# Kernel optimization log

Hardware: AMD Instinct MI355X
Metric: run time of the kernel (lower is better)

The kernel has to match this reference:

```python
import jax, jax.numpy as jnp
import numpy as np

B, N, E, H = 1, 4096, 2048, 16
D = E // H  # head_size = 128
DEGREE = 4
LN_EPS = 1e-5
ROPE_BASE = 10000.0


def rope_cos_sin(n, d):
    # [n, d//2] tables
    inv_freq = 1.0 / (ROPE_BASE ** (jnp.arange(0, d, 2, dtype=jnp.float32) / d))
    t = jnp.arange(n, dtype=jnp.float32)[:, None] * inv_freq[None, :]
    return jnp.cos(t), jnp.sin(t)


def apply_rope(x, cos, sin):
    # x: [b, n, h, d]; rotate-half RoPE
    x1, x2 = jnp.split(x, 2, axis=-1)
    c = cos[None, :, None, :]
    s = sin[None, :, None, :]
    return jnp.concatenate([x1 * c - x2 * s, x1 * s + x2 * c], axis=-1)


def layernorm(x, scale, bias, eps=LN_EPS):
    m = jnp.mean(x, axis=-1, keepdims=True)
    v = jnp.var(x, axis=-1, keepdims=True)
    return (x - m) * jax.lax.rsqrt(v + eps) * scale + bias


def polynomial_attention(q, k, v, degree, is_causal):
    # q,k,v: [b, h, n, d]
    a = jnp.einsum('bhnd,bhmd->bhnm', q, k) ** degree
    if is_causal:
        a = jnp.tril(a)
    denom = jnp.sum(a, axis=-1, keepdims=True)
    return jnp.einsum('bhnm,bhmd->bhnd', a / denom, v)


def setup_inputs() -> dict:
    key = jax.random.key(0)
    k0, k1, k2 = jax.random.split(key, 3)
    x = jax.random.normal(k0, (B, N, E), dtype=jnp.float32)
    # Dense(3*emb_dim, use_bias=False) and Dense(emb_dim, use_bias=False)
    w_qkv = jax.random.normal(k1, (E, 3 * E), dtype=jnp.float32) * (1.0 / np.sqrt(E))
    w_out = jax.random.normal(k2, (E, E), dtype=jnp.float32) * (1.0 / np.sqrt(E))
    # shared pre-attention LayerNorm over head dim (flax init: scale=1, bias=0)
    ln_scale = jnp.ones((D,), dtype=jnp.float32)
    ln_bias = jnp.zeros((D,), dtype=jnp.float32)
    return {"x": x, "w_qkv": w_qkv, "w_out": w_out,
            "ln_scale": ln_scale, "ln_bias": ln_bias}


def reference(x, w_qkv, w_out, ln_scale, ln_bias):
    b, n, e = x.shape
    proj = x @ w_qkv                              # [b, n, 3e]
    q, k, v = jnp.split(proj, 3, axis=-1)
    q = q.reshape(b, n, H, D)
    k = k.reshape(b, n, H, D)
    v = v.reshape(b, n, H, D)
    cos, sin = rope_cos_sin(n, D)
    q = apply_rope(q, cos, sin)
    k = apply_rope(k, cos, sin)
    # transpose branch (non-softmax): [b, h, n, d]
    q = q.transpose(0, 2, 1, 3)
    k = k.transpose(0, 2, 1, 3)
    v = v.transpose(0, 2, 1, 3)
    # shared pre_attn LayerNorm applied to q and k
    q = layernorm(q, ln_scale, ln_bias)
    k = layernorm(k, ln_scale, ln_bias)
    out = polynomial_attention(q, k, v, DEGREE, True)  # [b, h, n, d]
    out = out.transpose(0, 2, 1, 3).reshape(b, n, e)
    out = out @ w_out                              # dropout rate 0 / inference: identity
    return out
```

## Files before the change

### kernel.cpp

```cpp
#include <hip/hip_runtime.h>
#include <stdint.h>
#include <math.h>

#define N_SEQ 4096
#define EDIM  2048
#define NH    16
#define HD    128

typedef __attribute__((ext_vector_type(8))) short bf16x8;
typedef __attribute__((ext_vector_type(4))) float f32x4;

#define AS1 __attribute__((address_space(1)))
#define AS3 __attribute__((address_space(3)))

__device__ __forceinline__ void gll16(const unsigned short* g, unsigned short* l) {
    __builtin_amdgcn_global_load_lds((const AS1 unsigned int*)g,
                                     (AS3 unsigned int*)l, 16, 0, 0);
}

__device__ __forceinline__ unsigned short f2bf(float f) {
    union { float f; unsigned u; } v; v.f = f;
    unsigned r = v.u + 0x7FFFu + ((v.u >> 16) & 1u);
    return (unsigned short)(r >> 16);
}
__device__ __forceinline__ float bf2f(unsigned short h) {
    union { unsigned u; float f; } v; v.u = ((unsigned)h) << 16;
    return v.f;
}

__global__ void k_convert_x(const float* __restrict__ x,
                            unsigned short* __restrict__ xb, int n4) {
    int i = blockIdx.x * blockDim.x + threadIdx.x;
    int stride = gridDim.x * blockDim.x;
    for (; i < n4; i += stride) {
        float4 v = ((const float4*)x)[i];
        ushort4 o;
        o.x = f2bf(v.x); o.y = f2bf(v.y); o.z = f2bf(v.z); o.w = f2bf(v.w);
        ((ushort4*)xb)[i] = o;
    }
}

__global__ void k_transpose_f32_bf16(const float* __restrict__ in,
                                     unsigned short* __restrict__ out,
                                     int R, int C) {
    __shared__ unsigned short Ls[64][68];
    const int c0 = blockIdx.x * 64, r0 = blockIdx.y * 64;
    const int t = threadIdx.x;
    #pragma unroll
    for (int i = 0; i < 4; ++i) {
        int ch = i * 256 + t;
        int r = ch >> 4, c4 = (ch & 15) * 4;
        float4 v = *(const float4*)&in[(size_t)(r0 + r) * C + c0 + c4];
        ushort4 o;
        o.x = f2bf(v.x); o.y = f2bf(v.y); o.z = f2bf(v.z); o.w = f2bf(v.w);
        *(ushort4*)&Ls[r][c4] = o;
    }
    __syncthreads();
    #pragma unroll
    for (int i = 0; i < 2; ++i) {
        int ch = i * 256 + t;
        int rr = ch >> 3, c8 = (ch & 7) * 8;
        unsigned short vals[8];
        #pragma unroll
        for (int j = 0; j < 8; ++j) vals[j] = Ls[c8 + j][rr];
        uint4 pk;
        pk.x = (unsigned)vals[0] | ((unsigned)vals[1] << 16);
        pk.y = (unsigned)vals[2] | ((unsigned)vals[3] << 16);
        pk.z = (unsigned)vals[4] | ((unsigned)vals[5] << 16);
        pk.w = (unsigned)vals[6] | ((unsigned)vals[7] << 16);
        *(uint4*)&out[(size_t)(c0 + rr) * R + r0 + c8] = pk;
    }
}

template<int F32OUT>
__launch_bounds__(256, 2)
__global__ void k_gemm_bt(const unsigned short* __restrict__ A,
                          const unsigned short* __restrict__ Bt,
                          void* __restrict__ C,
                          int M, int N, int K) {
    __shared__ unsigned short sh[2 * 128 * 64];
    unsigned short* As = sh;
    unsigned short* Bs = sh + 128 * 64;

    const int t = threadIdx.x;
    const int wave = t >> 6, lane = t & 63;
    const int wm = wave >> 1, wn = wave & 1;
    const int lg = lane >> 4, lr = lane & 15;

    const int nbx = gridDim.x;
    const int nwg = nbx * gridDim.y;
    int bid = blockIdx.y * nbx + blockIdx.x;
    int swz = (bid & 7) * (nwg >> 3) + (bid >> 3);
    const int m0 = (swz / nbx) * 128;
    const int n0 = (swz % nbx) * 128;

    const unsigned short* aptr = A  + (size_t)m0 * K;
    const unsigned short* bptr = Bt + (size_t)n0 * K;

    f32x4 acc[4][4];
    #pragma unroll
    for (int i = 0; i < 4; ++i)
        #pragma unroll
        for (int j = 0; j < 4; ++j) acc[i][j] = f32x4{0.f, 0.f, 0.f, 0.f};

    int schr[4], srow[4], scb[4];
    #pragma unroll
    for (int i = 0; i < 4; ++i) {
        int ch = (i * 4 + wave) * 64 + lane;
        schr[i] = ch;
        srow[i] = ch >> 3;
        scb[i]  = (ch & 7) ^ ((ch >> 3) & 7);
    }

    const int nkb = K >> 6;
    for (int kb = 0; kb < nkb; ++kb) {
        __syncthreads();
        #pragma unroll
        for (int i = 0; i < 4; ++i) {
            const size_t goff = (size_t)srow[i] * K + (size_t)kb * 64 + scb[i] * 8;
            gll16(&aptr[goff], &As[schr[i] * 8]);
            gll16(&bptr[goff], &Bs[schr[i] * 8]);
        }
        __syncthreads();

        #pragma unroll
        for (int kk = 0; kk < 2; ++kk) {
            bf16x8 af[4], bf[4];
            const int cbx = ((kk * 4 + lg) ^ (lr & 7)) * 8;
            #pragma unroll
            for (int i = 0; i < 4; ++i) {
                af[i] = *(const bf16x8*)&As[(wm * 64 + i * 16 + lr) * 64 + cbx];
                bf[i] = *(const bf16x8*)&Bs[(wn * 64 + i * 16 + lr) * 64 + cbx];
            }
            #pragma unroll
            for (int i = 0; i < 4; ++i)
                #pragma unroll
                for (int j = 0; j < 4; ++j)
                    acc[i][j] = __builtin_amdgcn_mfma_f32_16x16x32_bf16(af[i], bf[j], acc[i][j], 0, 0, 0);
        }
    }

    if (F32OUT) {
        #pragma unroll
        for (int i = 0; i < 4; ++i) {
            int row0 = m0 + wm * 64 + i * 16 + lg * 4;
            #pragma unroll
            for (int j = 0; j < 4; ++j) {
                int col = n0 + wn * 64 + j * 16 + lr;
                #pragma unroll
                for (int r = 0; r < 4; ++r)
                    ((float*)C)[(size_t)(row0 + r) * N + col] = acc[i][j][r];
            }
        }
    } else {
        __syncthreads();
        unsigned short* Cs = sh;
        #pragma unroll
        for (int i = 0; i < 4; ++i) {
            #pragma unroll
            for (int j = 0; j < 4; ++j) {
                int col = wn * 64 + j * 16 + lr;
                #pragma unroll
                for (int r = 0; r < 4; ++r)
                    Cs[(wm * 64 + i * 16 + lg * 4 + r) * 128 + col] = f2bf(acc[i][j][r]);
            }
        }
        __syncthreads();
        #pragma unroll
        for (int i = 0; i < 8; ++i) {
            int ch = i * 256 + t;
            int row = ch >> 4, c8 = (ch & 15) * 8;
            *(uint4*)&((unsigned short*)C)[(size_t)(m0 + row) * N + n0 + c8] =
                *(const uint4*)&Cs[row * 128 + c8];
        }
    }
}

__global__ void k_ropeln(const unsigned short* __restrict__ proj,
                         const float* __restrict__ ln_scale,
                         const float* __restrict__ ln_bias,
                         unsigned short* __restrict__ Qh,
                         unsigned short* __restrict__ Kh) {
    const int n = blockIdx.x;
    const int wave = threadIdx.x >> 6, lane = threadIdx.x & 63;
    float inv = expf(-((float)(2 * lane) / 128.0f) * 9.210340371976184f);
    float ang = (float)n * inv;
    float c = cosf(ang), s = sinf(ang);
    const float sc1 = ln_scale[lane], sc2 = ln_scale[lane + 64];
    const float b1 = ln_bias[lane],  b2 = ln_bias[lane + 64];

    for (int r = wave; r < 32; r += 4) {
        int h = r >> 1, qk = r & 1;
        const unsigned short* src = proj + (size_t)n * (3 * EDIM) + qk * EDIM + h * HD;
        float x1 = bf2f(src[lane]), x2 = bf2f(src[lane + 64]);
        float o1 = x1 * c - x2 * s;
        float o2 = x1 * s + x2 * c;
        float sum = o1 + o2, sq = o1 * o1 + o2 * o2;
        #pragma unroll
        for (int d = 1; d < 64; d <<= 1) {
            sum += __shfl_xor(sum, d);
            sq  += __shfl_xor(sq, d);
        }
        float mean = sum * (1.0f / 128.0f);
        float var = sq * (1.0f / 128.0f) - mean * mean;
        float rstd = rsqrtf(var + 1e-5f);
        float y1 = (o1 - mean) * rstd * sc1 + b1;
        float y2 = (o2 - mean) * rstd * sc2 + b2;
        unsigned short* dst = (qk ? Kh : Qh) + ((size_t)h * N_SEQ + n) * HD;
        dst[lane]      = f2bf(y1);
        dst[lane + 64] = f2bf(y2);
    }
}

__global__ void k_vtrans(const unsigned short* __restrict__ proj,
                         unsigned short* __restrict__ Vt) {
    __shared__ unsigned short Ls[64][136];
    const int h = blockIdx.y;
    const int n0 = blockIdx.x * 64;
    const int t = threadIdx.x;
    #pragma unroll
    for (int i = 0; i < 4; ++i) {
        int ch = i * 256 + t;
        int r = ch >> 4, d0 = (ch & 15) * 8;
        uint4 v = *(const uint4*)&proj[(size_t)(n0 + r) * (3 * EDIM) + 2 * EDIM + h * HD + d0];
        *(uint4*)&Ls[r][d0] = v;
    }
    __syncthreads();
    #pragma unroll
    for (int i = 0; i < 4; ++i) {
        int ch = i * 256 + t;
        int d = ch >> 3, p = ch & 7;
        unsigned short vals[8];
        #pragma unroll
        for (int j = 0; j < 8; ++j) {
            int ko = 32 * (p >> 2) + 16 * (j >> 2) + 4 * (p & 3) + (j & 3);
            vals[j] = Ls[ko][d];
        }
        uint4 pk;
        pk.x = (unsigned)vals[0] | ((unsigned)vals[1] << 16);
        pk.y = (unsigned)vals[2] | ((unsigned)vals[3] << 16);
        pk.z = (unsigned)vals[4] | ((unsigned)vals[5] << 16);
        pk.w = (unsigned)vals[6] | ((unsigned)vals[7] << 16);
        *(uint4*)&Vt[((size_t)h * HD + d) * N_SEQ + n0 + p * 8] = pk;
    }
}

__launch_bounds__(256, 2)
__global__ void k_attn(const unsigned short* __restrict__ Qh,
                       const unsigned short* __restrict__ Kh,
                       const unsigned short* __restrict__ Vt,
                       unsigned short* __restrict__ O) {
    __shared__ unsigned short pool[4 * 8192];

    const int t = threadIdx.x;
    const int w = t >> 6, lane = t & 63;
    const int wq = w >> 1, wk = w & 1;
    const int lg = lane >> 4, lr = lane & 15;

    const int b = blockIdx.x;
    const int h = (b & 7) * 2 + ((b >> 3) & 1);
    const int qt = 63 - (b >> 4);
    const int q0 = qt * 64;
    const int qbase = q0 + wq * 32;
    const int kbase = wk * 32;

    bf16x8 qf[2][4];
    #pragma unroll
    for (int mi = 0; mi < 2; ++mi)
        #pragma unroll
        for (int kk = 0; kk < 4; ++kk)
            qf[mi][kk] = *(const bf16x8*)&Qh[((size_t)h * N_SEQ + qbase + mi * 16 + lr) * HD + kk * 32 + lg * 8];

    f32x4 acc[2][8];
    #pragma unroll
    for (int i = 0; i < 2; ++i)
        #pragma unroll
        for (int j = 0; j < 8; ++j) acc[i][j] = f32x4{0.f, 0.f, 0.f, 0.f};
    f32x4 accd[2];
    accd[0] = f32x4{0.f, 0.f, 0.f, 0.f};
    accd[1] = f32x4{0.f, 0.f, 0.f, 0.f};

    bf16x8 onesf;
    {
        short ov = (lr == 0) ? (short)0x3F80 : (short)0;
        #pragma unroll
        for (int j = 0; j < 8; ++j) onesf[j] = ov;
    }

    int kch[4], vch[4];
    const unsigned short* kg[4];
    const unsigned short* vg[4];
    #pragma unroll
    for (int i = 0; i < 4; ++i) {
        int ch = i * 256 + t;
        kch[i] = ch;
        int r = ch >> 4, p = ch & 15;
        int csrc = (p & 8) | ((p ^ r) & 7);
        kg[i] = Kh + ((size_t)h * N_SEQ + r) * HD + csrc * 8;
    }
    #pragma unroll
    for (int i = 0; i < 4; ++i) {
        int ch = i * 256 + t;
        vch[i] = ch;
        int d = ch >> 3, p2 = ch & 7;
        int c2src = (p2 ^ d) & 7;
        vg[i] = Vt + ((size_t)h * HD + d) * N_SEQ + c2src * 8;
    }

    const int nkb = qt + 1;

    union U8 { unsigned u[4]; bf16x8 v; };

    auto stage = [&](unsigned short* Kn, unsigned short* Vn) {
        #pragma unroll
        for (int i = 0; i < 4; ++i) { gll16(kg[i], Kn + kch[i] * 8); kg[i] += 64 * HD; }
        #pragma unroll
        for (int i = 0; i < 4; ++i) { gll16(vg[i], Vn + vch[i] * 8); vg[i] += 64; }
    };

    auto compute = [&](int k0, const unsigned short* Kc, const unsigned short* Vc) {
        if (k0 + kbase > qbase + 31) return;
        f32x4 sa[2][2];
        #pragma unroll
        for (int i = 0; i < 2; ++i) {
            sa[i][0] = f32x4{0.f, 0.f, 0.f, 0.f};
            sa[i][1] = f32x4{0.f, 0.f, 0.f, 0.f};
        }
        bf16x8 kf[2][4];
        #pragma unroll
        for (int nj = 0; nj < 2; ++nj)
            #pragma unroll
            for (int kk = 0; kk < 4; ++kk) {
                int row = kbase + nj * 16 + lr;
                int c = kk * 4 + lg;
                int cs = (c & 8) | ((c ^ row) & 7);
                kf[nj][kk] = *(const bf16x8*)&Kc[row * 128 + cs * 8];
            }
        __builtin_amdgcn_s_setprio(1);
        #pragma unroll
        for (int kk = 0; kk < 4; ++kk)
            #pragma unroll
            for (int nj = 0; nj < 2; ++nj)
                #pragma unroll
                for (int mi = 0; mi < 2; ++mi)
                    sa[mi][nj] = __builtin_amdgcn_mfma_f32_16x16x32_bf16(
                        kf[nj][kk], qf[mi][kk], sa[mi][nj], 0, 0, 0);
        __builtin_amdgcn_s_setprio(0);

        unsigned wreg[2][2][2];
        const bool nomask = (k0 + kbase + 31 <= qbase);
        #pragma unroll
        for (int mi = 0; mi < 2; ++mi)
            #pragma unroll
            for (int nj = 0; nj < 2; ++nj) {
                float p[4];
                #pragma unroll
                for (int r = 0; r < 4; ++r) {
                    float sv = sa[mi][nj][r];
                    float t2 = sv * sv;
                    p[r] = t2 * t2;
                    if (!nomask) {
                        int gk = k0 + kbase + nj * 16 + lg * 4 + r;
                        int gq = qbase + mi * 16 + lr;
                        p[r] = (gk <= gq) ? p[r] : 0.0f;
                    }
                }
                asm("v_cvt_pk_bf16_f32 %0, %1, %2" : "=v"(wreg[mi][nj][0]) : "v"(p[0]), "v"(p[1]));
                asm("v_cvt_pk_bf16_f32 %0, %1, %2" : "=v"(wreg[mi][nj][1]) : "v"(p[2]), "v"(p[3]));
            }

        bf16x8 pa[2];
        #pragma unroll
        for (int mi = 0; mi < 2; ++mi) {
            U8 u;
            u.u[0] = wreg[mi][0][0];
            u.u[1] = wreg[mi][0][1];
            u.u[2] = wreg[mi][1][0];
            u.u[3] = wreg[mi][1][1];
            pa[mi] = u.v;
        }
        __builtin_amdgcn_s_setprio(1);
        #pragma unroll
        for (int ni = 0; ni < 8; ++ni) {
            int d = ni * 16 + lr;
            int cs = ((wk * 4 + lg) ^ (d & 7)) & 7;
            bf16x8 vf = *(const bf16x8*)&Vc[d * 64 + cs * 8];
            #pragma unroll
            for (int mi = 0; mi < 2; ++mi)
                acc[mi][ni] = __builtin_amdgcn_mfma_f32_16x16x32_bf16(pa[mi], vf, acc[mi][ni], 0, 0, 0);
        }
        #pragma unroll
        for (int mi = 0; mi < 2; ++mi)
            accd[mi] = __builtin_amdgcn_mfma_f32_16x16x32_bf16(pa[mi], onesf, accd[mi], 0, 0, 0);
        __builtin_amdgcn_s_setprio(0);
    };

    stage(pool, pool + 16384);
    int kb0 = 0;
    if (nkb & 1) {
        asm volatile("s_waitcnt vmcnt(0)" ::: "memory");
        __builtin_amdgcn_s_barrier();
        compute(0, pool, pool + 16384);
        __builtin_amdgcn_s_barrier();
        if (nkb > 1) stage(pool, pool + 16384);
        kb0 = 1;
    }
    for (int kb = kb0; kb < nkb; kb += 2) {
        stage(pool + 8192, pool + 16384 + 8192);
        asm volatile("s_waitcnt vmcnt(8)" ::: "memory");
        __builtin_amdgcn_s_barrier();
        compute(kb * 64, pool, pool + 16384);
        __builtin_amdgcn_s_barrier();
        if (kb + 2 < nkb) {
            stage(pool, pool + 16384);
            asm volatile("s_waitcnt vmcnt(8)" ::: "memory");
        } else {
            asm volatile("s_waitcnt vmcnt(0)" ::: "memory");
        }
        __builtin_amdgcn_s_barrier();
        compute((kb + 1) * 64, pool + 8192, pool + 16384 + 8192);
        __builtin_amdgcn_s_barrier();
    }

    asm volatile("s_waitcnt vmcnt(0)" ::: "memory");
    __syncthreads();
    float* Xf = (float*)pool;
    const int xbase = wq * 4608 + lane * 4;
    if (wk == 1) {
        #pragma unroll
        for (int mi = 0; mi < 2; ++mi) {
            #pragma unroll
            for (int ni = 0; ni < 8; ++ni)
                *(f32x4*)&Xf[xbase + (mi * 8 + ni) * 256] = acc[mi][ni];
            *(f32x4*)&Xf[xbase + (16 + mi) * 256] = accd[mi];
        }
    }
    __syncthreads();
    unsigned short* Cs = pool + 20480;
    if (wk == 0) {
        #pragma unroll
        for (int mi = 0; mi < 2; ++mi) {
            #pragma unroll
            for (int ni = 0; ni < 8; ++ni) {
                f32x4 o = *(const f32x4*)&Xf[xbase + (mi * 8 + ni) * 256];
                acc[mi][ni][0] += o[0]; acc[mi][ni][1] += o[1];
                acc[mi][ni][2] += o[2]; acc[mi][ni][3] += o[3];
            }
            f32x4 od = *(const f32x4*)&Xf[xbase + (16 + mi) * 256];
            accd[mi][0] += od[0]; accd[mi][1] += od[1];
            accd[mi][2] += od[2]; accd[mi][3] += od[3];
        }
        #pragma unroll
        for (int mi = 0; mi < 2; ++mi) {
            #pragma unroll
            for (int r = 0; r < 4; ++r) {
                float dv = __shfl(accd[mi][r], lane & 48);
                float rinv = 1.0f / dv;
                int rw = wq * 32 + mi * 16 + lg * 4 + r;
                #pragma unroll
                for (int ni = 0; ni < 8; ++ni)
                    Cs[rw * 128 + ni * 16 + lr] = f2bf(acc[mi][ni][r] * rinv);
            }
        }
    }
    __syncthreads();
    #pragma unroll
    for (int i = 0; i < 4; ++i) {
        int ch = i * 256 + t;
        int row = ch >> 4, c8 = (ch & 15) * 8;
        *(uint4*)&O[(size_t)(q0 + row) * EDIM + h * HD + c8] = *(const uint4*)&Cs[row * 128 + c8];
    }
}

extern "C" void kernel_launch(void* const* d_in, const int* in_sizes, int n_in,
                              void* d_out, int out_size, void* d_ws, size_t ws_size,
                              hipStream_t stream) {
    const float* x        = (const float*)d_in[0];
    const float* w_qkv    = (const float*)d_in[1];
    const float* w_out    = (const float*)d_in[2];
    const float* ln_scale = (const float*)d_in[3];
    const float* ln_bias  = (const float*)d_in[4];

    if (ws_size < 134217728u) return;

    char* ws = (char*)d_ws;
    unsigned short* xb    = (unsigned short*)(ws);
    unsigned short* wqkvT = (unsigned short*)(ws + 16777216);
    unsigned short* woutT = (unsigned short*)(ws + 41943040);
    unsigned short* proj  = (unsigned short*)(ws + 50331648);
    unsigned short* Kh    = (unsigned short*)(ws + 100663296);
    unsigned short* Vt    = (unsigned short*)(ws + 117440512);
    unsigned short* Qh    = wqkvT;
    unsigned short* attnO = xb;

    k_convert_x<<<2048, 256, 0, stream>>>(x, xb, (N_SEQ * EDIM) / 4);
    k_transpose_f32_bf16<<<dim3(3 * EDIM / 64, EDIM / 64), 256, 0, stream>>>(w_qkv, wqkvT, EDIM, 3 * EDIM);
    k_transpose_f32_bf16<<<dim3(EDIM / 64, EDIM / 64), 256, 0, stream>>>(w_out, woutT, EDIM, EDIM);
    k_gemm_bt<0><<<dim3(3 * EDIM / 128, N_SEQ / 128), 256, 0, stream>>>(xb, wqkvT, proj, N_SEQ, 3 * EDIM, EDIM);
    k_ropeln<<<N_SEQ, 256, 0, stream>>>(proj, ln_scale, ln_bias, Qh, Kh);
    k_vtrans<<<dim3(N_SEQ / 64, NH), 256, 0, stream>>>(proj, Vt);
    k_attn<<<1024, 256, 0, stream>>>(Qh, Kh, Vt, attnO);
    k_gemm_bt<1><<<dim3(EDIM / 128, N_SEQ / 128), 256, 0, stream>>>(attnO, woutT, (float*)d_out, N_SEQ, EDIM, EDIM);
}
```

Baseline: 286.3 us.

## Double attention query tile to 128 rows and reorder block scheduling

The attention kernel now processes 128 query rows per block (64 per wave pair) instead of 64, halving the grid to 512 blocks and reusing each staged K/V tile across twice as many queries. Block order is split into two batches, the first longest-first and the second shortest-first, to balance causal work across CUs. The cross-wave reduction is done in two passes to fit the larger accumulator set in LDS. The cost is much higher register pressure from doubled accumulators and Q fragments, which may lower occupancy under the 2-blocks launch bound.

```diff
diff --git a/kernel.cpp b/kernel.cpp
--- a/kernel.cpp
+++ b/kernel.cpp
@@ -257,28 +257,30 @@
     const int wq = w >> 1, wk = w & 1;
     const int lg = lane >> 4, lr = lane & 15;
 
-    const int b = blockIdx.x;
-    const int h = (b & 7) * 2 + ((b >> 3) & 1);
-    const int qt = 63 - (b >> 4);
-    const int q0 = qt * 64;
-    const int qbase = q0 + wq * 32;
+    const int s = blockIdx.x & 255;
+    const int batch = blockIdx.x >> 8;
+    const int h = (s & 7) * 2 + ((s >> 3) & 1);
+    const int qq = s >> 4;
+    const int qt = batch ? qq : (31 - qq);
+    const int q0 = qt * 128;
+    const int qbase = q0 + wq * 64;
     const int kbase = wk * 32;
 
-    bf16x8 qf[2][4];
-    #pragma unroll
-    for (int mi = 0; mi < 2; ++mi)
+    bf16x8 qf[4][4];
+    #pragma unroll
+    for (int mi = 0; mi < 4; ++mi)
         #pragma unroll
         for (int kk = 0; kk < 4; ++kk)
             qf[mi][kk] = *(const bf16x8*)&Qh[((size_t)h * N_SEQ + qbase + mi * 16 + lr) * HD + kk * 32 + lg * 8];
 
-    f32x4 acc[2][8];
-    #pragma unroll
-    for (int i = 0; i < 2; ++i)
+    f32x4 acc[4][8];
+    #pragma unroll
+    for (int i = 0; i < 4; ++i)
         #pragma unroll
         for (int j = 0; j < 8; ++j) acc[i][j] = f32x4{0.f, 0.f, 0.f, 0.f};
-    f32x4 accd[2];
-    accd[0] = f32x4{0.f, 0.f, 0.f, 0.f};
-    accd[1] = f32x4{0.f, 0.f, 0.f, 0.f};
+    f32x4 accd[4];
+    #pragma unroll
+    for (int i = 0; i < 4; ++i) accd[i] = f32x4{0.f, 0.f, 0.f, 0.f};
 
     bf16x8 onesf;
     {
@@ -307,7 +309,7 @@
         vg[i] = Vt + ((size_t)h * HD + d) * N_SEQ + c2src * 8;
     }
 
-    const int nkb = qt + 1;
+    const int nkb = 2 * qt + 2;
 
     union U8 { unsigned u[4]; bf16x8 v; };
 
@@ -319,38 +321,37 @@
     };
 
     auto compute = [&](int k0, const unsigned short* Kc, const unsigned short* Vc) {
-        if (k0 + kbase > qbase + 31) return;
-        f32x4 sa[2][2];
-        #pragma unroll
-        for (int i = 0; i < 2; ++i) {
+        if (k0 + kbase > qbase + 63) return;
+        f32x4 sa[4][2];
+        #pragma unroll
+        for (int i = 0; i < 4; ++i) {
             sa[i][0] = f32x4{0.f, 0.f, 0.f, 0.f};
             sa[i][1] = f32x4{0.f, 0.f, 0.f, 0.f};
         }
-        bf16x8 kf[2][4];
-        #pragma unroll
-        for (int nj = 0; nj < 2; ++nj)
+        #pragma unroll
+        for (int nj = 0; nj < 2; ++nj) {
+            bf16x8 kf4[4];
             #pragma unroll
             for (int kk = 0; kk < 4; ++kk) {
                 int row = kbase + nj * 16 + lr;
                 int c = kk * 4 + lg;
                 int cs = (c & 8) | ((c ^ row) & 7);
-                kf[nj][kk] = *(const bf16x8*)&Kc[row * 128 + cs * 8];
-            }
-        __builtin_amdgcn_s_setprio(1);
-        #pragma unroll
-        for (int kk = 0; kk < 4; ++kk)
-            #pragma unroll
-            for (int nj = 0; nj < 2; ++nj)
-                #pragma unroll
-                for (int mi = 0; mi < 2; ++mi)
+                kf4[kk] = *(const bf16x8*)&Kc[row * 128 + cs * 8];
+            }
+            __builtin_amdgcn_s_setprio(1);
+            #pragma unroll
+            for (int kk = 0; kk < 4; ++kk)
+                #pragma unroll
+                for (int mi = 0; mi < 4; ++mi)
                     sa[mi][nj] = __builtin_amdgcn_mfma_f32_16x16x32_bf16(
-                        kf[nj][kk], qf[mi][kk], sa[mi][nj], 0, 0, 0);
-        __builtin_amdgcn_s_setprio(0);
-
-        unsigned wreg[2][2][2];
+                        kf4[kk], qf[mi][kk], sa[mi][nj], 0, 0, 0);
+            __builtin_amdgcn_s_setprio(0);
+        }
+
+        unsigned wreg[4][2][2];
         const bool nomask = (k0 + kbase + 31 <= qbase);
         #pragma unroll
-        for (int mi = 0; mi < 2; ++mi)
+        for (int mi = 0; mi < 4; ++mi)
             #pragma unroll
             for (int nj = 0; nj < 2; ++nj) {
                 float p[4];
@@ -369,9 +370,9 @@
                 asm("v_cvt_pk_bf16_f32 %0, %1, %2" : "=v"(wreg[mi][nj][1]) : "v"(p[2]), "v"(p[3]));
             }
 
-        bf16x8 pa[2];
-        #pragma unroll
-        for (int mi = 0; mi < 2; ++mi) {
+        bf16x8 pa[4];
+        #pragma unroll
+        for (int mi = 0; mi < 4; ++mi) {
             U8 u;
             u.u[0] = wreg[mi][0][0];
             u.u[1] = wreg[mi][0][1];
@@ -386,26 +387,18 @@
             int cs = ((wk * 4 + lg) ^ (d & 7)) & 7;
             bf16x8 vf = *(const bf16x8*)&Vc[d * 64 + cs * 8];
             #pragma unroll
-            for (int mi = 0; mi < 2; ++mi)
+            for (int mi = 0; mi < 4; ++mi)
                 acc[mi][ni] = __builtin_amdgcn_mfma_f32_16x16x32_bf16(pa[mi], vf, acc[mi][ni], 0, 0, 0);
         }
         #pragma unroll
-        for (int mi = 0; mi < 2; ++mi)
+        for (int mi = 0; mi < 4; ++mi)
             accd[mi] = __builtin_amdgcn_mfma_f32_16x16x32_bf16(pa[mi], onesf, accd[mi], 0, 0, 0);
         __builtin_amdgcn_s_setprio(0);
     };
 
     stage(pool, pool + 16384);
-    int kb0 = 0;
-    if (nkb & 1) {
-        asm volatile("s_waitcnt vmcnt(0)" ::: "memory");
-        __builtin_amdgcn_s_barrier();
-        compute(0, pool, pool + 16384);
-        __builtin_amdgcn_s_barrier();
-        if (nkb > 1) stage(pool, pool + 16384);
-        kb0 = 1;
-    }
-    for (int kb = kb0; kb < nkb; kb += 2) {
+
+    for (int kb = 0; kb < nkb; kb += 2) {
         stage(pool + 8192, pool + 16384 + 8192);
         asm volatile("s_waitcnt vmcnt(8)" ::: "memory");
         __builtin_amdgcn_s_barrier();
@@ -423,40 +416,46 @@
     }
 
     asm volatile("s_waitcnt vmcnt(0)" ::: "memory");
-    __syncthreads();
     float* Xf = (float*)pool;
     const int xbase = wq * 4608 + lane * 4;
-    if (wk == 1) {
-        #pragma unroll
-        for (int mi = 0; mi < 2; ++mi) {
-            #pragma unroll
-            for (int ni = 0; ni < 8; ++ni)
-                *(f32x4*)&Xf[xbase + (mi * 8 + ni) * 256] = acc[mi][ni];
-            *(f32x4*)&Xf[xbase + (16 + mi) * 256] = accd[mi];
+    #pragma unroll
+    for (int p = 0; p < 2; ++p) {
+        __syncthreads();
+        if (wk == 1) {
+            #pragma unroll
+            for (int i = 0; i < 2; ++i) {
+                #pragma unroll
+                for (int ni = 0; ni < 8; ++ni)
+                    *(f32x4*)&Xf[xbase + (i * 8 + ni) * 256] = acc[p * 2 + i][ni];
+                *(f32x4*)&Xf[xbase + (16 + i) * 256] = accd[p * 2 + i];
+            }
+        }
+        __syncthreads();
+        if (wk == 0) {
+            #pragma unroll
+            for (int i = 0; i < 2; ++i) {
+                #pragma unroll
+                for (int ni = 0; ni < 8; ++ni) {
+                    f32x4 o = *(const f32x4*)&Xf[xbase + (i * 8 + ni) * 256];
+                    acc[p * 2 + i][ni][0] += o[0]; acc[p * 2 + i][ni][1] += o[1];
+                    acc[p * 2 + i][ni][2] += o[2]; acc[p * 2 + i][ni][3] += o[3];
+                }
+                f32x4 od = *(const f32x4*)&Xf[xbase + (16 + i) * 256];
+                accd[p * 2 + i][0] += od[0]; accd[p * 2 + i][1] += od[1];
+                accd[p * 2 + i][2] += od[2]; accd[p * 2 + i][3] += od[3];
+            }
         }
     }
     __syncthreads();
-    unsigned short* Cs = pool + 20480;
+    unsigned short* Cs = pool;
     if (wk == 0) {
         #pragma unroll
-        for (int mi = 0; mi < 2; ++mi) {
-            #pragma unroll
-            for (int ni = 0; ni < 8; ++ni) {
-                f32x4 o = *(const f32x4*)&Xf[xbase + (mi * 8 + ni) * 256];
-                acc[mi][ni][0] += o[0]; acc[mi][ni][1] += o[1];
-                acc[mi][ni][2] += o[2]; acc[mi][ni][3] += o[3];
-            }
-            f32x4 od = *(const f32x4*)&Xf[xbase + (16 + mi) * 256];
-            accd[mi][0] += od[0]; accd[mi][1] += od[1];
-            accd[mi][2] += od[2]; accd[mi][3] += od[3];
-        }
-        #pragma unroll
-        for (int mi = 0; mi < 2; ++mi) {
+        for (int mi = 0; mi < 4; ++mi) {
             #pragma unroll
             for (int r = 0; r < 4; ++r) {
                 float dv = __shfl(accd[mi][r], lane & 48);
                 float rinv = 1.0f / dv;
-                int rw = wq * 32 + mi * 16 + lg * 4 + r;
+                int rw = wq * 64 + mi * 16 + lg * 4 + r;
                 #pragma unroll
                 for (int ni = 0; ni < 8; ++ni)
                     Cs[rw * 128 + ni * 16 + lr] = f2bf(acc[mi][ni][r] * rinv);
@@ -465,7 +464,7 @@
     }
     __syncthreads();
     #pragma unroll
-    for (int i = 0; i < 4; ++i) {
+    for (int i = 0; i < 8; ++i) {
         int ch = i * 256 + t;
         int row = ch >> 4, c8 = (ch & 15) * 8;
         *(uint4*)&O[(size_t)(q0 + row) * EDIM + h * HD + c8] = *(const uint4*)&Cs[row * 128 + c8];
@@ -499,6 +498,6 @@
     k_gemm_bt<0><<<dim3(3 * EDIM / 128, N_SEQ / 128), 256, 0, stream>>>(xb, wqkvT, proj, N_SEQ, 3 * EDIM, EDIM);
     k_ropeln<<<N_SEQ, 256, 0, stream>>>(proj, ln_scale, ln_bias, Qh, Kh);
     k_vtrans<<<dim3(N_SEQ / 64, NH), 256, 0, stream>>>(proj, Vt);
-    k_attn<<<1024, 256, 0, stream>>>(Qh, Kh, Vt, attnO);
+    k_attn<<<512, 256, 0, stream>>>(Qh, Kh, Vt, attnO);
     k_gemm_bt<1><<<dim3(EDIM / 128, N_SEQ / 128), 256, 0, stream>>>(attnO, woutT, (float*)d_out, N_SEQ, EDIM, EDIM);
 }
```

After: 538.1 us. 87.9% more time.

## Rewrite GEMM as 8-wave 256x128 tile with triple-buffered async LDS pipeline

Applied to the files above, without the earlier changes.

Replaces the 4-wave 128x128 GEMM with an 8-wave kernel covering 256x128 tiles. K-tiles are staged into three LDS buffers, two tiles ahead, using split async global-to-LDS loads and explicit vmcnt waits, with raised wave priority around the MFMA blocks. The goal is to hide global load latency behind matrix math and remove the two full barriers per K step. This costs 144KB of LDS per block, which may limit occupancy despite the launch bound of 2. It also relies on hand-tuned waitcnt counts being correct.

```diff
diff --git a/kernel.cpp b/kernel.cpp
--- a/kernel.cpp
+++ b/kernel.cpp
@@ -73,17 +73,15 @@
 }
 
 template<int F32OUT>
-__launch_bounds__(256, 2)
-__global__ void k_gemm_bt(const unsigned short* __restrict__ A,
-                          const unsigned short* __restrict__ Bt,
-                          void* __restrict__ C,
-                          int M, int N, int K) {
-    __shared__ unsigned short sh[2 * 128 * 64];
-    unsigned short* As = sh;
-    unsigned short* Bs = sh + 128 * 64;
-
-    const int t = threadIdx.x;
-    const int wave = t >> 6, lane = t & 63;
+__launch_bounds__(512, 2)
+__global__ void k_gemm8p(const unsigned short* __restrict__ A,
+                         const unsigned short* __restrict__ Bt,
+                         void* __restrict__ C,
+                         int M, int N, int K) {
+    __shared__ unsigned short pool[73728];
+
+    const int tid = threadIdx.x;
+    const int wave = tid >> 6, lane = tid & 63;
     const int wm = wave >> 1, wn = wave & 1;
     const int lg = lane >> 4, lr = lane & 15;
 
@@ -91,11 +89,27 @@
     const int nwg = nbx * gridDim.y;
     int bid = blockIdx.y * nbx + blockIdx.x;
     int swz = (bid & 7) * (nwg >> 3) + (bid >> 3);
-    const int m0 = (swz / nbx) * 128;
+    const int m0 = (swz / nbx) * 256;
     const int n0 = (swz % nbx) * 128;
 
-    const unsigned short* aptr = A  + (size_t)m0 * K;
-    const unsigned short* bptr = Bt + (size_t)n0 * K;
+    int ach[4], bch[2];
+    const unsigned short *Ag[4], *Bg[2];
+    #pragma unroll
+    for (int i = 0; i < 4; ++i) {
+        int ch = i * 512 + tid;
+        ach[i] = ch;
+        int r = ch >> 3, p = ch & 7;
+        int csrc = (p ^ (r & 7)) & 7;
+        Ag[i] = A + (size_t)(m0 + r) * K + csrc * 8;
+    }
+    #pragma unroll
+    for (int i = 0; i < 2; ++i) {
+        int ch = i * 512 + tid;
+        bch[i] = ch;
+        int r = ch >> 3, p = ch & 7;
+        int csrc = (p ^ (r & 7)) & 7;
+        Bg[i] = Bt + (size_t)(n0 + r) * K + csrc * 8;
+    }
 
     f32x4 acc[4][4];
     #pragma unroll
@@ -103,72 +117,98 @@
         #pragma unroll
         for (int j = 0; j < 4; ++j) acc[i][j] = f32x4{0.f, 0.f, 0.f, 0.f};
 
-    int schr[4], srow[4], scb[4];
-    #pragma unroll
-    for (int i = 0; i < 4; ++i) {
-        int ch = (i * 4 + wave) * 64 + lane;
-        schr[i] = ch;
-        srow[i] = ch >> 3;
-        scb[i]  = (ch & 7) ^ ((ch >> 3) & 7);
-    }
-
-    const int nkb = K >> 6;
-    for (int kb = 0; kb < nkb; ++kb) {
-        __syncthreads();
-        #pragma unroll
-        for (int i = 0; i < 4; ++i) {
-            const size_t goff = (size_t)srow[i] * K + (size_t)kb * 64 + scb[i] * 8;
-            gll16(&aptr[goff], &As[schr[i] * 8]);
-            gll16(&bptr[goff], &Bs[schr[i] * 8]);
-        }
-        __syncthreads();
-
-        #pragma unroll
-        for (int kk = 0; kk < 2; ++kk) {
-            bf16x8 af[4], bf[4];
-            const int cbx = ((kk * 4 + lg) ^ (lr & 7)) * 8;
-            #pragma unroll
-            for (int i = 0; i < 4; ++i) {
-                af[i] = *(const bf16x8*)&As[(wm * 64 + i * 16 + lr) * 64 + cbx];
-                bf[i] = *(const bf16x8*)&Bs[(wn * 64 + i * 16 + lr) * 64 + cbx];
-            }
-            #pragma unroll
-            for (int i = 0; i < 4; ++i)
-                #pragma unroll
-                for (int j = 0; j < 4; ++j)
-                    acc[i][j] = __builtin_amdgcn_mfma_f32_16x16x32_bf16(af[i], bf[j], acc[i][j], 0, 0, 0);
-        }
+    bf16x8 af[4], bf[4];
+    auto rdA = [&](const unsigned short* Cb, int kk) {
+        const int cs = ((kk * 4 + lg) ^ (lr & 7)) & 7;
+        #pragma unroll
+        for (int j = 0; j < 4; ++j)
+            af[j] = *(const bf16x8*)&Cb[(wm * 64 + j * 16 + lr) * 64 + cs * 8];
+    };
+    auto rdB = [&](const unsigned short* Cb, int kk) {
+        const int cs = ((kk * 4 + lg) ^ (lr & 7)) & 7;
+        #pragma unroll
+        for (int n = 0; n < 4; ++n)
+            bf[n] = *(const bf16x8*)&Cb[16384 + (wn * 64 + n * 16 + lr) * 64 + cs * 8];
+    };
+    auto mm16 = [&]() {
+        __builtin_amdgcn_s_setprio(1);
+        #pragma unroll
+        for (int j = 0; j < 4; ++j)
+            #pragma unroll
+            for (int n = 0; n < 4; ++n)
+                acc[j][n] = __builtin_amdgcn_mfma_f32_16x16x32_bf16(
+                    af[j], bf[n], acc[j][n], 0, 0, 0);
+        __builtin_amdgcn_s_setprio(0);
+    };
+    auto stageFull = [&](int T, unsigned short* buf) {
+        #pragma unroll
+        for (int i = 0; i < 4; ++i) gll16(Ag[i] + (size_t)T * 64, buf + ach[i] * 8);
+        #pragma unroll
+        for (int i = 0; i < 2; ++i) gll16(Bg[i] + (size_t)T * 64, buf + 16384 + bch[i] * 8);
+    };
+    auto stageH1 = [&](int T, unsigned short* buf) {
+        gll16(Ag[0] + (size_t)T * 64, buf + ach[0] * 8);
+        gll16(Ag[1] + (size_t)T * 64, buf + ach[1] * 8);
+        gll16(Bg[0] + (size_t)T * 64, buf + 16384 + bch[0] * 8);
+    };
+    auto stageH2 = [&](int T, unsigned short* buf) {
+        gll16(Ag[2] + (size_t)T * 64, buf + ach[2] * 8);
+        gll16(Ag[3] + (size_t)T * 64, buf + ach[3] * 8);
+        gll16(Bg[1] + (size_t)T * 64, buf + 16384 + bch[1] * 8);
+    };
+
+    const int NT = K >> 6;
+
+    stageFull(0, pool);
+    stageFull(1, pool + 24576);
+
+    int bt = 0, bs = 2;
+    for (int t = 0; t < NT; ++t) {
+        unsigned short* Cb = pool + bt * 24576;
+        unsigned short* Sb = pool + bs * 24576;
+        const bool pre = (t + 2 < NT);
+        if (pre) stageH1(t + 2, Sb);
+        if (pre)                asm volatile("s_waitcnt vmcnt(9)" ::: "memory");
+        else if (t + 1 < NT)    asm volatile("s_waitcnt vmcnt(6)" ::: "memory");
+        else                    asm volatile("s_waitcnt vmcnt(0)" ::: "memory");
+        __builtin_amdgcn_s_barrier();
+
+        rdA(Cb, 0); rdB(Cb, 0);
+        mm16();
+        if (pre) stageH2(t + 2, Sb);
+        rdA(Cb, 1); rdB(Cb, 1);
+        mm16();
+        __builtin_amdgcn_s_barrier();
+        bt = (bt == 2) ? 0 : bt + 1;
+        bs = (bs == 2) ? 0 : bs + 1;
     }
 
     if (F32OUT) {
         #pragma unroll
-        for (int i = 0; i < 4; ++i) {
-            int row0 = m0 + wm * 64 + i * 16 + lg * 4;
-            #pragma unroll
-            for (int j = 0; j < 4; ++j) {
-                int col = n0 + wn * 64 + j * 16 + lr;
+        for (int j = 0; j < 4; ++j) {
+            int row0 = m0 + wm * 64 + j * 16 + lg * 4;
+            #pragma unroll
+            for (int n = 0; n < 4; ++n) {
+                int col = n0 + wn * 64 + n * 16 + lr;
                 #pragma unroll
                 for (int r = 0; r < 4; ++r)
-                    ((float*)C)[(size_t)(row0 + r) * N + col] = acc[i][j][r];
+                    ((float*)C)[(size_t)(row0 + r) * N + col] = acc[j][n][r];
             }
         }
     } else {
-        __syncthreads();
-        unsigned short* Cs = sh;
-        #pragma unroll
-        for (int i = 0; i < 4; ++i) {
-            #pragma unroll
-            for (int j = 0; j < 4; ++j) {
-                int col = wn * 64 + j * 16 + lr;
+        unsigned short* Cs = pool;
+        #pragma unroll
+        for (int j = 0; j < 4; ++j)
+            #pragma unroll
+            for (int n = 0; n < 4; ++n)
                 #pragma unroll
                 for (int r = 0; r < 4; ++r)
-                    Cs[(wm * 64 + i * 16 + lg * 4 + r) * 128 + col] = f2bf(acc[i][j][r]);
-            }
-        }
+                    Cs[(wm * 64 + j * 16 + lg * 4 + r) * 128 + wn * 64 + n * 16 + lr] =
+                        f2bf(acc[j][n][r]);
         __syncthreads();
         #pragma unroll
         for (int i = 0; i < 8; ++i) {
-            int ch = i * 256 + t;
+            int ch = i * 512 + tid;
             int row = ch >> 4, c8 = (ch & 15) * 8;
             *(uint4*)&((unsigned short*)C)[(size_t)(m0 + row) * N + n0 + c8] =
                 *(const uint4*)&Cs[row * 128 + c8];
@@ -275,7 +315,7 @@
     #pragma unroll
     for (int i = 0; i < 2; ++i)
         #pragma unroll
-        for (int j = 0; j < 8; ++j) acc[i][j] = f32x4{0.f, 0.f, 0.f, 0.f};
+        for (int j2 = 0; j2 < 8; ++j2) acc[i][j2] = f32x4{0.f, 0.f, 0.f, 0.f};
     f32x4 accd[2];
     accd[0] = f32x4{0.f, 0.f, 0.f, 0.f};
     accd[1] = f32x4{0.f, 0.f, 0.f, 0.f};
@@ -284,7 +324,7 @@
     {
         short ov = (lr == 0) ? (short)0x3F80 : (short)0;
         #pragma unroll
-        for (int j = 0; j < 8; ++j) onesf[j] = ov;
+        for (int j2 = 0; j2 < 8; ++j2) onesf[j2] = ov;
     }
 
     int kch[4], vch[4];
@@ -496,9 +536,9 @@
     k_convert_x<<<2048, 256, 0, stream>>>(x, xb, (N_SEQ * EDIM) / 4);
     k_transpose_f32_bf16<<<dim3(3 * EDIM / 64, EDIM / 64), 256, 0, stream>>>(w_qkv, wqkvT, EDIM, 3 * EDIM);
     k_transpose_f32_bf16<<<dim3(EDIM / 64, EDIM / 64), 256, 0, stream>>>(w_out, woutT, EDIM, EDIM);
-    k_gemm_bt<0><<<dim3(3 * EDIM / 128, N_SEQ / 128), 256, 0, stream>>>(xb, wqkvT, proj, N_SEQ, 3 * EDIM, EDIM);
+    k_gemm8p<0><<<dim3(3 * EDIM / 128, N_SEQ / 256), 512, 0, stream>>>(xb, wqkvT, proj, N_SEQ, 3 * EDIM, EDIM);
     k_ropeln<<<N_SEQ, 256, 0, stream>>>(proj, ln_scale, ln_bias, Qh, Kh);
     k_vtrans<<<dim3(N_SEQ / 64, NH), 256, 0, stream>>>(proj, Vt);
     k_attn<<<1024, 256, 0, stream>>>(Qh, Kh, Vt, attnO);
-    k_gemm_bt<1><<<dim3(EDIM / 128, N_SEQ / 128), 256, 0, stream>>>(attnO, woutT, (float*)d_out, N_SEQ, EDIM, EDIM);
-}
+    k_gemm8p<1><<<dim3(EDIM / 128, N_SEQ / 256), 512, 0, stream>>>(attnO, woutT, (float*)d_out, N_SEQ, EDIM, EDIM);
+}
```

Measured after the change: 269.0 us. 6.1% less time.
